# Optimization experiments

Measured on AMD Instinct MI355X. Metric: run time of the kernel, lower is better.

Reference implementation:

```python
import jax
import jax.numpy as jnp
import numpy as np
from jax import lax

GAMMA = 0.99  # cfg.offline_gamma
TAU = 0.95    # cfg.tau (GAE lambda)
T = 4_194_304  # trajectory length (many episodes concatenated, separated by mask=0)


def setup_inputs() -> dict:
    key = jax.random.key(0)
    k1, k2, k3, k4 = jax.random.split(key, 4)
    rewards = jax.random.normal(k1, (T, 1), dtype=jnp.float32)
    values = jax.random.normal(k2, (T, 1), dtype=jnp.float32)        # critic.get_max_value(states)
    next_values = jax.random.normal(k3, (T, 1), dtype=jnp.float32)   # critic.get_max_value(next_states) (bootstrap=True)
    masks = jax.random.randint(k4, (T, 1), 0, 2).astype(jnp.int32)   # 1 = non-terminal, 0 = episode end
    return {"rewards": rewards, "values": values, "next_values": next_values, "masks": masks}


def reference(rewards, values, next_values, masks):
    """Faithful translation of A2C.get_phi's reversed loop as a single lax.scan.

    returns[i]    = r[i] + gamma * (prev_return * m[i] + (1 - m[i]) * next_values[i])
    deltas[i]     = r[i] + gamma * prev_value * m[i] - values[i]
    advantages[i] = deltas[i] + gamma * tau * prev_advantage * m[i]
    with prev_* taken from step i+1 (zeros past the end).
    """
    m = masks.astype(rewards.dtype)  # [T,1]

    def step(carry, xs):
        prev_ret, prev_val, prev_adv = carry  # each [1]
        r, v, nv, mm = xs                     # each [1]
        ret = r + GAMMA * (prev_ret * mm + (1.0 - mm) * nv)
        delta = r + GAMMA * prev_val * mm - v
        adv = delta + GAMMA * TAU * prev_adv * mm
        return (ret, v, adv), (adv, ret)

    zero = jnp.zeros((1,), dtype=rewards.dtype)
    init = (zero, zero, zero)
    _, (advantages, returns) = lax.scan(
        step, init, (rewards, values, next_values, m), reverse=True
    )
    return advantages, returns  # each [T,1]
```

## Files before the change

kernel.cpp:

```cpp
#include <hip/hip_runtime.h>

#define GAMMA 0.99f
#define TAU   0.95f
#define GTAU  (GAMMA * TAU)

constexpr int SEQ   = 4;
constexpr int BLK   = 256;
constexpr int CHUNK = BLK * SEQ;

__device__ __forceinline__ void post_compose(float& A, float& B, float rA, float rB) {
    B = fmaf(A, rB, B);
    A *= rA;
}
__device__ __forceinline__ void pre_compose(float& A, float& B, float lA, float lB) {
    B = fmaf(lA, B, lB);
    A *= lA;
}

__global__ __launch_bounds__(BLK) void k_fused1(
    const float* __restrict__ r, const float* __restrict__ v,
    const float* __restrict__ nv, const int* __restrict__ m,
    float* __restrict__ out_adv, float* __restrict__ out_ret, int T)
{
    const int  tid  = threadIdx.x;
    const int  lane = tid & 63;
    const int  w    = tid >> 6;
    const int  c    = (int)blockIdx.x;
    const long base = (long)c * CHUNK + (long)tid * SEQ;
    const long p    = (long)(c + 1) * CHUNK;

    __shared__ float wSum[4][4];
    __shared__ float s_cb[2];

    float pm = 0.f, pr = 0.f, pv = 0.f, pv1 = 0.f, pnv = 0.f;
    if (w == 0 && p < (long)T) {
        long i = p + lane;
        if (i < (long)T) {
            pm  = (float)m[i];
            pr  = r[i];
            pv  = v[i];
            pv1 = (i + 1 < (long)T) ? v[i + 1] : 0.f;
            pnv = nv[i];
        }
    }

    float delta[SEQ], dd[SEQ];
    unsigned vbits = 0, mbits = 0;
    float Aa = 1.f, Ba = 0.f, Ar = 1.f, Br = 0.f;

    const bool wfull = ((long)c * CHUNK + (long)(w + 1) * 64 * SEQ) <= (long)T;

    if (wfull) {
        vbits = 0xFu;
        float4 r4 = *(const float4*)(r  + base);
        float4 v4 = *(const float4*)(v  + base);
        float4 n4 = *(const float4*)(nv + base);
        int4   m4 = *(const int4*)  (m  + base);
        float vnext = __shfl_down(v4.x, 1);
        if (lane == 63) vnext = (base + SEQ < (long)T) ? v[base + SEQ] : 0.f;

        float rr[4]  = {r4.x, r4.y, r4.z, r4.w};
        float vv[5]  = {v4.x, v4.y, v4.z, v4.w, vnext};
        float nn[4]  = {n4.x, n4.y, n4.z, n4.w};
        float fmv[4] = {(float)m4.x, (float)m4.y, (float)m4.z, (float)m4.w};
        #pragma unroll
        for (int i = SEQ - 1; i >= 0; --i) {
            if (fmv[i] != 0.f) mbits |= (1u << i);
            delta[i] = rr[i] + GAMMA * fmv[i] * vv[i+1] - vv[i];
            dd[i]    = rr[i] + GAMMA * (1.f - fmv[i]) * nn[i];
            pre_compose(Aa, Ba, GTAU  * fmv[i], delta[i]);
            pre_compose(Ar, Br, GAMMA * fmv[i], dd[i]);
        }
    } else {
        #pragma unroll
        for (int ii = 0; ii < SEQ; ++ii) {
            int i = SEQ - 1 - ii;
            long idx = base + i;
            bool val = idx < (long)T;
            float rr  = val ? r[idx]  : 0.f;
            float vv0 = val ? v[idx]  : 0.f;
            float vv1 = (idx + 1 < (long)T) ? v[idx + 1] : 0.f;
            float nn  = val ? nv[idx] : 0.f;
            float fmv = val ? (float)m[idx] : 0.f;
            if (val) vbits |= (1u << i);
            if (val && fmv != 0.f) mbits |= (1u << i);
            delta[i] = val ? (rr + GAMMA * fmv * vv1 - vv0) : 0.f;
            dd[i]    = val ? (rr + GAMMA * (1.f - fmv) * nn) : 0.f;
            pre_compose(Aa, Ba, val ? GTAU * fmv  : 1.f, delta[i]);
            pre_compose(Ar, Br, val ? GAMMA * fmv : 1.f, dd[i]);
        }
    }

    #pragma unroll
    for (int st = 1; st < 64; st <<= 1) {
        float oAa = __shfl_down(Aa, st);
        float oBa = __shfl_down(Ba, st);
        float oAr = __shfl_down(Ar, st);
        float oBr = __shfl_down(Br, st);
        if (lane + st < 64) {
            post_compose(Aa, Ba, oAa, oBa);
            post_compose(Ar, Br, oAr, oBr);
        }
    }
    float eAa = __shfl_down(Aa, 1);
    float eBa = __shfl_down(Ba, 1);
    float eAr = __shfl_down(Ar, 1);
    float eBr = __shfl_down(Br, 1);
    if (lane == 63) { eAa=1.f; eBa=0.f; eAr=1.f; eBr=0.f; }

    if (lane == 0) { wSum[w][0]=Aa; wSum[w][1]=Ba; wSum[w][2]=Ar; wSum[w][3]=Br; }
    __syncthreads();

    float WAa=1.f, WBa=0.f, WAr=1.f, WBr=0.f;
    for (int j = 3; j > w; --j) {
        pre_compose(WAa, WBa, wSum[j][0], wSum[j][1]);
        pre_compose(WAr, WBr, wSum[j][2], wSum[j][3]);
    }

    if (w == 0) {
        float MAa=1.f, MBa=0.f, MAr=1.f, MBr=0.f;
        if (p < (long)T) {
            {
                long i = p + lane;
                bool have = i < (long)T;
                float aA=1.f, aB=0.f, rA_=1.f, rB_=0.f;
                if (have) {
                    aA  = GTAU * pm;
                    aB  = pr + GAMMA * pm * pv1 - pv;
                    rA_ = GAMMA * pm;
                    rB_ = pr + GAMMA * (1.f - pm) * pnv;
                }
                bool term = (!have) || (pm == 0.f);
                unsigned long long bz = __ballot(term);
                #pragma unroll
                for (int st = 1; st < 64; st <<= 1) {
                    float oAa = __shfl_down(aA,  st);
                    float oBa = __shfl_down(aB,  st);
                    float oAr = __shfl_down(rA_, st);
                    float oBr = __shfl_down(rB_, st);
                    if (lane + st < 64) {
                        post_compose(aA,  aB,  oAa, oBa);
                        post_compose(rA_, rB_, oAr, oBr);
                    }
                }
                MAa = __shfl(aA, 0);  MBa = __shfl(aB, 0);
                MAr = __shfl(rA_, 0); MBr = __shfl(rB_, 0);
                if (bz != 0ull) goto carry_done;
            }
            for (long jb = p + 64; ; jb += 64) {
                long i = jb + lane;
                bool have = i < (long)T;
                float aA=1.f, aB=0.f, rA_=1.f, rB_=0.f;
                float mi = 0.f;
                if (have) {
                    mi = (float)m[i];
                    float ri  = r[i];
                    float vi  = v[i];
                    float vi1 = (i + 1 < (long)T) ? v[i + 1] : 0.f;
                    float nvi = nv[i];
                    aA  = GTAU * mi;
                    aB  = ri + GAMMA * mi * vi1 - vi;
                    rA_ = GAMMA * mi;
                    rB_ = ri + GAMMA * (1.f - mi) * nvi;
                }
                bool term = (!have) || (mi == 0.f);
                unsigned long long bz = __ballot(term);
                #pragma unroll
                for (int st = 1; st < 64; st <<= 1) {
                    float oAa = __shfl_down(aA,  st);
                    float oBa = __shfl_down(aB,  st);
                    float oAr = __shfl_down(rA_, st);
                    float oBr = __shfl_down(rB_, st);
                    if (lane + st < 64) {
                        post_compose(aA,  aB,  oAa, oBa);
                        post_compose(rA_, rB_, oAr, oBr);
                    }
                }
                float bAa = __shfl(aA, 0),  bBa = __shfl(aB, 0);
                float bAr = __shfl(rA_, 0), bBr = __shfl(rB_, 0);
                post_compose(MAa, MBa, bAa, bBa);
                post_compose(MAr, MBr, bAr, bBr);
                if (bz != 0ull) break;
            }
        }
carry_done:
        if (lane == 0) {
            s_cb[0] = MBa;
            s_cb[1] = MBr;
        }
    }
    __syncthreads();
    const float cbA = s_cb[0];
    const float cbR = s_cb[1];

    float xa = fmaf(WAa, cbA, WBa);
    float xr = fmaf(WAr, cbR, WBr);
    xa = fmaf(eAa, xa, eBa);
    xr = fmaf(eAr, xr, eBr);

    if (wfull) {
        float ta[4], tr[4];
        #pragma unroll
        for (int i = SEQ - 1; i >= 0; --i) {
            float a  = (mbits >> i & 1u) ? GTAU  : 0.f;
            float cc = (mbits >> i & 1u) ? GAMMA : 0.f;
            xa = fmaf(a,  xa, delta[i]);
            xr = fmaf(cc, xr, dd[i]);
            ta[i] = xa; tr[i] = xr;
        }
        *(float4*)(out_adv + base) = make_float4(ta[0], ta[1], ta[2], ta[3]);
        *(float4*)(out_ret + base) = make_float4(tr[0], tr[1], tr[2], tr[3]);
    } else {
        #pragma unroll
        for (int i = SEQ - 1; i >= 0; --i) {
            bool val = (vbits >> i) & 1u;
            float a  = val ? ((mbits >> i & 1u) ? GTAU  : 0.f) : 1.f;
            float cc = val ? ((mbits >> i & 1u) ? GAMMA : 0.f) : 1.f;
            xa = fmaf(a,  xa, delta[i]);
            xr = fmaf(cc, xr, dd[i]);
            if (base + i < (long)T) {
                out_adv[base + i] = xa;
                out_ret[base + i] = xr;
            }
        }
    }
}

extern "C" void kernel_launch(void* const* d_in, const int* in_sizes, int n_in,
                              void* d_out, int out_size, void* d_ws, size_t ws_size,
                              hipStream_t stream) {
    const float* r  = (const float*)d_in[0];
    const float* v  = (const float*)d_in[1];
    const float* nv = (const float*)d_in[2];
    const int*   m  = (const int*)d_in[3];
    const int T = in_sizes[0];
    const int nblk = (T + CHUNK - 1) / CHUNK;

    float* out_adv = (float*)d_out;
    float* out_ret = (float*)d_out + T;

    k_fused1<<<nblk, BLK, 0, stream>>>(r, v, nv, m, out_adv, out_ret, T);
}
```

Baseline: 24.23 us.

## Make each wavefront an independent chunk and drop block-level barriers

New measurement: 22.82 us. 1.06x faster.

```diff
diff --git a/kernel.cpp b/kernel.cpp
--- a/kernel.cpp
+++ b/kernel.cpp
@@ -4,9 +4,9 @@
 #define TAU   0.95f
 #define GTAU  (GAMMA * TAU)
 
-constexpr int SEQ   = 4;
-constexpr int BLK   = 256;
-constexpr int CHUNK = BLK * SEQ;
+constexpr int WSEQ   = 4;
+constexpr int WCHUNK = 64 * WSEQ;
+constexpr int BLK    = 256;
 
 __device__ __forceinline__ void post_compose(float& A, float& B, float rA, float rB) {
     B = fmaf(A, rB, B);
@@ -17,23 +17,21 @@
     A *= lA;
 }
 
-__global__ __launch_bounds__(BLK) void k_fused1(
+__global__ __launch_bounds__(BLK) void k_wave(
     const float* __restrict__ r, const float* __restrict__ v,
     const float* __restrict__ nv, const int* __restrict__ m,
-    float* __restrict__ out_adv, float* __restrict__ out_ret, int T)
+    float* __restrict__ out_adv, float* __restrict__ out_ret, int T, int nchunk)
 {
-    const int  tid  = threadIdx.x;
-    const int  lane = tid & 63;
-    const int  w    = tid >> 6;
-    const int  c    = (int)blockIdx.x;
-    const long base = (long)c * CHUNK + (long)tid * SEQ;
-    const long p    = (long)(c + 1) * CHUNK;
-
-    __shared__ float wSum[4][4];
-    __shared__ float s_cb[2];
+    const int  lane  = threadIdx.x & 63;
+    const int  w     = threadIdx.x >> 6;
+    const int  chunk = (int)blockIdx.x * 4 + w;
+    if (chunk >= nchunk) return;
+
+    const long base = (long)chunk * WCHUNK + (long)lane * WSEQ;
+    const long p    = (long)(chunk + 1) * WCHUNK;
 
     float pm = 0.f, pr = 0.f, pv = 0.f, pv1 = 0.f, pnv = 0.f;
-    if (w == 0 && p < (long)T) {
+    if (p < (long)T) {
         long i = p + lane;
         if (i < (long)T) {
             pm  = (float)m[i];
@@ -44,27 +42,27 @@
         }
     }
 
-    float delta[SEQ], dd[SEQ];
+    float delta[WSEQ], dd[WSEQ];
     unsigned vbits = 0, mbits = 0;
     float Aa = 1.f, Ba = 0.f, Ar = 1.f, Br = 0.f;
-
-    const bool wfull = ((long)c * CHUNK + (long)(w + 1) * 64 * SEQ) <= (long)T;
-
-    if (wfull) {
+    const bool full = (p <= (long)T);
+
+    if (full) {
         vbits = 0xFu;
         float4 r4 = *(const float4*)(r  + base);
         float4 v4 = *(const float4*)(v  + base);
         float4 n4 = *(const float4*)(nv + base);
         int4   m4 = *(const int4*)  (m  + base);
+        float vhi   = __shfl(pv, 0);
         float vnext = __shfl_down(v4.x, 1);
-        if (lane == 63) vnext = (base + SEQ < (long)T) ? v[base + SEQ] : 0.f;
+        if (lane == 63) vnext = vhi;
 
         float rr[4]  = {r4.x, r4.y, r4.z, r4.w};
         float vv[5]  = {v4.x, v4.y, v4.z, v4.w, vnext};
         float nn[4]  = {n4.x, n4.y, n4.z, n4.w};
         float fmv[4] = {(float)m4.x, (float)m4.y, (float)m4.z, (float)m4.w};
         #pragma unroll
-        for (int i = SEQ - 1; i >= 0; --i) {
+        for (int i = WSEQ - 1; i >= 0; --i) {
             if (fmv[i] != 0.f) mbits |= (1u << i);
             delta[i] = rr[i] + GAMMA * fmv[i] * vv[i+1] - vv[i];
             dd[i]    = rr[i] + GAMMA * (1.f - fmv[i]) * nn[i];
@@ -73,8 +71,8 @@
         }
     } else {
         #pragma unroll
-        for (int ii = 0; ii < SEQ; ++ii) {
-            int i = SEQ - 1 - ii;
+        for (int ii = 0; ii < WSEQ; ++ii) {
+            int i = WSEQ - 1 - ii;
             long idx = base + i;
             bool val = idx < (long)T;
             float rr  = val ? r[idx]  : 0.f;
@@ -108,100 +106,83 @@
     float eBr = __shfl_down(Br, 1);
     if (lane == 63) { eAa=1.f; eBa=0.f; eAr=1.f; eBr=0.f; }
 
-    if (lane == 0) { wSum[w][0]=Aa; wSum[w][1]=Ba; wSum[w][2]=Ar; wSum[w][3]=Br; }
-    __syncthreads();
-
-    float WAa=1.f, WBa=0.f, WAr=1.f, WBr=0.f;
-    for (int j = 3; j > w; --j) {
-        pre_compose(WAa, WBa, wSum[j][0], wSum[j][1]);
-        pre_compose(WAr, WBr, wSum[j][2], wSum[j][3]);
-    }
-
-    if (w == 0) {
-        float MAa=1.f, MBa=0.f, MAr=1.f, MBr=0.f;
-        if (p < (long)T) {
-            {
-                long i = p + lane;
-                bool have = i < (long)T;
-                float aA=1.f, aB=0.f, rA_=1.f, rB_=0.f;
-                if (have) {
-                    aA  = GTAU * pm;
-                    aB  = pr + GAMMA * pm * pv1 - pv;
-                    rA_ = GAMMA * pm;
-                    rB_ = pr + GAMMA * (1.f - pm) * pnv;
+    float cbA = 0.f, cbR = 0.f;
+    if (p < (long)T) {
+        float MAa, MBa, MAr, MBr;
+        {
+            long i = p + lane;
+            bool have = i < (long)T;
+            float aA=1.f, aB=0.f, rA_=1.f, rB_=0.f;
+            if (have) {
+                aA  = GTAU * pm;
+                aB  = pr + GAMMA * pm * pv1 - pv;
+                rA_ = GAMMA * pm;
+                rB_ = pr + GAMMA * (1.f - pm) * pnv;
+            }
+            bool term = (!have) || (pm == 0.f);
+            unsigned long long bz = __ballot(term);
+            #pragma unroll
+            for (int st = 1; st < 64; st <<= 1) {
+                float oAa = __shfl_down(aA,  st);
+                float oBa = __shfl_down(aB,  st);
+                float oAr = __shfl_down(rA_, st);
+                float oBr = __shfl_down(rB_, st);
+                if (lane + st < 64) {
+                    post_compose(aA,  aB,  oAa, oBa);
+                    post_compose(rA_, rB_, oAr, oBr);
                 }
-                bool term = (!have) || (pm == 0.f);
-                unsigned long long bz = __ballot(term);
-                #pragma unroll
-                for (int st = 1; st < 64; st <<= 1) {
-                    float oAa = __shfl_down(aA,  st);
-                    float oBa = __shfl_down(aB,  st);
-                    float oAr = __shfl_down(rA_, st);
-                    float oBr = __shfl_down(rB_, st);
-                    if (lane + st < 64) {
-                        post_compose(aA,  aB,  oAa, oBa);
-                        post_compose(rA_, rB_, oAr, oBr);
+            }
+            MAa = __shfl(aA, 0);  MBa = __shfl(aB, 0);
+            MAr = __shfl(rA_, 0); MBr = __shfl(rB_, 0);
+            if (bz == 0ull) {
+                for (long jb = p + 64; ; jb += 64) {
+                    long i2 = jb + lane;
+                    bool have2 = i2 < (long)T;
+                    float aA2=1.f, aB2=0.f, rA2=1.f, rB2=0.f;
+                    float mi = 0.f;
+                    if (have2) {
+                        mi = (float)m[i2];
+                        float ri  = r[i2];
+                        float vi  = v[i2];
+                        float vi1 = (i2 + 1 < (long)T) ? v[i2 + 1] : 0.f;
+                        float nvi = nv[i2];
+                        aA2 = GTAU * mi;
+                        aB2 = ri + GAMMA * mi * vi1 - vi;
+                        rA2 = GAMMA * mi;
+                        rB2 = ri + GAMMA * (1.f - mi) * nvi;
                     }
+                    bool term2 = (!have2) || (mi == 0.f);
+                    unsigned long long bz2 = __ballot(term2);
+                    #pragma unroll
+                    for (int st = 1; st < 64; st <<= 1) {
+                        float oAa = __shfl_down(aA2, st);
+                        float oBa = __shfl_down(aB2, st);
+                        float oAr = __shfl_down(rA2, st);
+                        float oBr = __shfl_down(rB2, st);
+                        if (lane + st < 64) {
+                            post_compose(aA2, aB2, oAa, oBa);
+                            post_compose(rA2, rB2, oAr, oBr);
+                        }
+                    }
+                    float bAa = __shfl(aA2, 0), bBa = __shfl(aB2, 0);
+                    float bAr = __shfl(rA2, 0), bBr = __shfl(rB2, 0);
+                    post_compose(MAa, MBa, bAa, bBa);
+                    post_compose(MAr, MBr, bAr, bBr);
+                    if (bz2 != 0ull) break;
                 }
-                MAa = __shfl(aA, 0);  MBa = __shfl(aB, 0);
-                MAr = __shfl(rA_, 0); MBr = __shfl(rB_, 0);
-                if (bz != 0ull) goto carry_done;
-            }
-            for (long jb = p + 64; ; jb += 64) {
-                long i = jb + lane;
-                bool have = i < (long)T;
-                float aA=1.f, aB=0.f, rA_=1.f, rB_=0.f;
-                float mi = 0.f;
-                if (have) {
-                    mi = (float)m[i];
-                    float ri  = r[i];
-                    float vi  = v[i];
-                    float vi1 = (i + 1 < (long)T) ? v[i + 1] : 0.f;
-                    float nvi = nv[i];
-                    aA  = GTAU * mi;
-                    aB  = ri + GAMMA * mi * vi1 - vi;
-                    rA_ = GAMMA * mi;
-                    rB_ = ri + GAMMA * (1.f - mi) * nvi;
-                }
-                bool term = (!have) || (mi == 0.f);
-                unsigned long long bz = __ballot(term);
-                #pragma unroll
-                for (int st = 1; st < 64; st <<= 1) {
-                    float oAa = __shfl_down(aA,  st);
-                    float oBa = __shfl_down(aB,  st);
-                    float oAr = __shfl_down(rA_, st);
-                    float oBr = __shfl_down(rB_, st);
-                    if (lane + st < 64) {
-                        post_compose(aA,  aB,  oAa, oBa);
-                        post_compose(rA_, rB_, oAr, oBr);
-                    }
-                }
-                float bAa = __shfl(aA, 0),  bBa = __shfl(aB, 0);
-                float bAr = __shfl(rA_, 0), bBr = __shfl(rB_, 0);
-                post_compose(MAa, MBa, bAa, bBa);
-                post_compose(MAr, MBr, bAr, bBr);
-                if (bz != 0ull) break;
-            }
-        }
-carry_done:
-        if (lane == 0) {
-            s_cb[0] = MBa;
-            s_cb[1] = MBr;
-        }
-    }
-    __syncthreads();
-    const float cbA = s_cb[0];
-    const float cbR = s_cb[1];
-
-    float xa = fmaf(WAa, cbA, WBa);
-    float xr = fmaf(WAr, cbR, WBr);
-    xa = fmaf(eAa, xa, eBa);
-    xr = fmaf(eAr, xr, eBr);
-
-    if (wfull) {
+            }
+        }
+        cbA = MBa;
+        cbR = MBr;
+    }
+
+    float xa = fmaf(eAa, cbA, eBa);
+    float xr = fmaf(eAr, cbR, eBr);
+
+    if (full) {
         float ta[4], tr[4];
         #pragma unroll
-        for (int i = SEQ - 1; i >= 0; --i) {
+        for (int i = WSEQ - 1; i >= 0; --i) {
             float a  = (mbits >> i & 1u) ? GTAU  : 0.f;
             float cc = (mbits >> i & 1u) ? GAMMA : 0.f;
             xa = fmaf(a,  xa, delta[i]);
@@ -212,7 +193,7 @@
         *(float4*)(out_ret + base) = make_float4(tr[0], tr[1], tr[2], tr[3]);
     } else {
         #pragma unroll
-        for (int i = SEQ - 1; i >= 0; --i) {
+        for (int i = WSEQ - 1; i >= 0; --i) {
             bool val = (vbits >> i) & 1u;
             float a  = val ? ((mbits >> i & 1u) ? GTAU  : 0.f) : 1.f;
             float cc = val ? ((mbits >> i & 1u) ? GAMMA : 0.f) : 1.f;
@@ -234,10 +215,11 @@
     const float* nv = (const float*)d_in[2];
     const int*   m  = (const int*)d_in[3];
     const int T = in_sizes[0];
-    const int nblk = (T + CHUNK - 1) / CHUNK;
+    const int nchunk = (T + WCHUNK - 1) / WCHUNK;
+    const int nblk   = (nchunk + 3) / 4;
 
     float* out_adv = (float*)d_out;
     float* out_ret = (float*)d_out + T;
 
-    k_fused1<<<nblk, BLK, 0, stream>>>(r, v, nv, m, out_adv, out_ret, T);
-}
+    k_wave<<<nblk, BLK, 0, stream>>>(r, v, nv, m, out_adv, out_ret, T, nchunk);
+}
```
